# Kernel optimization log

Measured on AMD Instinct MI355X. Metric: run time of the kernel, lower is better.

## Reference

```python
import jax, jax.numpy as jnp
import numpy as np

SCALE = 0.08838834764831845  # 1/sqrt(head_dim=128)
B, H, HKV, D = 32, 32, 8, 128
NUM_BLOCKS, BLOCK_SIZE, MAX_NUM_BLOCKS = 4096, 16, 256


def setup_inputs() -> dict:
    key = jax.random.key(0)
    ks = jax.random.split(key, 8)
    q = jax.random.normal(ks[0], (B, H, D), dtype=jnp.float32)
    k = jax.random.normal(ks[1], (B, HKV, D), dtype=jnp.float32)
    v = jax.random.normal(ks[2], (B, HKV, D), dtype=jnp.float32)
    k_cache = jax.random.normal(ks[3], (NUM_BLOCKS, BLOCK_SIZE, HKV, D), dtype=jnp.float32)
    v_cache = jax.random.normal(ks[4], (NUM_BLOCKS, BLOCK_SIZE, HKV, D), dtype=jnp.float32)
    slot_mapping = jax.random.randint(ks[5], (B,), 0, NUM_BLOCKS * BLOCK_SIZE, dtype=jnp.int32)
    block_tables = jax.random.randint(ks[6], (B, MAX_NUM_BLOCKS), 0, NUM_BLOCKS, dtype=jnp.int32)
    context_lens = jax.random.randint(ks[7], (B,), 0, MAX_NUM_BLOCKS * BLOCK_SIZE, dtype=jnp.int32)
    return {"q": q, "k": k, "v": v, "k_cache": k_cache, "v_cache": v_cache,
            "slot_mapping": slot_mapping, "block_tables": block_tables,
            "context_lens": context_lens}


def reference(q, k, v, k_cache, v_cache, slot_mapping, block_tables, context_lens):
    nb, bs, hkv, d = k_cache.shape
    b, h, _ = q.shape
    groups = h // hkv  # GQA repeat factor (repeat_interleave semantics)

    # --- store_kvcache: scatter the new decode token's k/v into the paged cache ---
    k_cache = k_cache.reshape(-1, hkv, d).at[slot_mapping].set(k).reshape(nb, bs, hkv, d)
    v_cache = v_cache.reshape(-1, hkv, d).at[slot_mapping].set(v).reshape(nb, bs, hkv, d)

    # --- block-table gather: [B, max_blocks] -> [B, T, HKV, D], T = max_blocks*bs ---
    t = block_tables.shape[1] * bs
    ids = jnp.maximum(block_tables, 0)  # clamp_min(0)
    k_tok = k_cache[ids].reshape(b, t, hkv, d)
    v_tok = v_cache[ids].reshape(b, t, hkv, d)

    # --- validity mask: block must be >=0 and token position < context_len ---
    pos = jnp.arange(t, dtype=jnp.int32)
    block_mask = jnp.repeat(block_tables >= 0, bs, axis=1)  # [B, T]
    valid = block_mask & (pos[None, :] < context_lens[:, None])
    has_tokens = valid.any(axis=1)  # [B]
    safe_valid = valid | ((~has_tokens)[:, None] & (pos[None, :] == 0))

    # --- attention (GQA via reshape instead of repeat_interleave materialization) ---
    qg = q.reshape(b, hkv, groups, d)  # head h = kv*groups + g matches repeat_interleave
    scores = jnp.einsum('bkgd,btkd->bkgt', qg, k_tok) * SCALE  # [B, HKV, G, T]
    scores = jnp.where(safe_valid[:, None, None, :], scores, -jnp.inf)
    w = jax.nn.softmax(scores.astype(jnp.float32), axis=-1).astype(q.dtype)
    o = jnp.einsum('bkgt,btkd->bkgd', w, v_tok).reshape(b, h, d)
    o = o * has_tokens[:, None, None].astype(o.dtype)
    return o[:, None, :, :]  # [B, 1, H, D] (matches transpose(1,2) of [B,H,1,D])
```

## Files before the change

### kernel.cpp

```cpp
#include <hip/hip_runtime.h>
#include <math.h>

#define B_ 32
#define H_ 32
#define HKV_ 8
#define G_ 4
#define D_ 128
#define BS_ 16
#define MAXNB_ 256
#define NPAGES_ 4096
#define NSLOTS_ (NPAGES_ * BS_)
#define SC_ (0.08838834764831845f * 1.4426950408889634f)
#define NEG_ -1e30f

__global__ void build_slot_map(const int* __restrict__ slot_mapping,
                               unsigned char* __restrict__ map,
                               unsigned int* __restrict__ pagemask) {
  const int tid = threadIdx.x;
  uint4* m4 = (uint4*)map;
#pragma unroll
  for (int i = 0; i < NSLOTS_ / 16 / 256; ++i)
    m4[tid + i * 256] = make_uint4(0u, 0u, 0u, 0u);
  uint4* p4 = (uint4*)pagemask;
#pragma unroll
  for (int i = 0; i < NPAGES_ * 4 / 16 / 256; ++i)
    p4[tid + i * 256] = make_uint4(0u, 0u, 0u, 0u);
  __syncthreads();
  if (tid == 0) {
#pragma unroll
    for (int j = 0; j < B_; ++j) {
      int s = slot_mapping[j];
      map[s] = (unsigned char)(j + 1);
      pagemask[s >> 4] |= (1u << (s & 15));
    }
  }
}

__global__ __launch_bounds__(256, 2) void attn_split(
    const float* __restrict__ q,
    const float* __restrict__ k_new,
    const float* __restrict__ v_new,
    const float* __restrict__ k_cache,
    const float* __restrict__ v_cache,
    const int* __restrict__ block_tables,
    const int* __restrict__ context_lens,
    const unsigned char* __restrict__ map,
    const unsigned int* __restrict__ pagemask,
    float* __restrict__ O_part,
    float* __restrict__ M_part,
    float* __restrict__ L_part,
    int nsplit)
{
  __shared__ float Ml[4][4];
  __shared__ float Ll[4][4];
  __shared__ float Ob[4][4][128];

  const int tid = threadIdx.x;
  const int tok = tid >> 4;
  const int c = tid & 15;

  const int s  = blockIdx.x % nsplit;
  const int bk = blockIdx.x / nsplit;
  const int kv = bk % HKV_;
  const int b  = bk / HKV_;

  float qr[G_][8];
#pragma unroll
  for (int g = 0; g < G_; ++g) {
    const float* qp = q + ((size_t)(b * H_ + kv * G_ + g)) * D_ + c * 8;
    float4 a0 = *(const float4*)qp;
    float4 a1 = *(const float4*)(qp + 4);
    qr[g][0] = a0.x * SC_; qr[g][1] = a0.y * SC_;
    qr[g][2] = a0.z * SC_; qr[g][3] = a0.w * SC_;
    qr[g][4] = a1.x * SC_; qr[g][5] = a1.y * SC_;
    qr[g][6] = a1.z * SC_; qr[g][7] = a1.w * SC_;
  }

  float m2[G_], l[G_], o[G_][8];
#pragma unroll
  for (int g = 0; g < G_; ++g) {
    m2[g] = NEG_; l[g] = 0.f;
#pragma unroll
    for (int j = 0; j < 8; ++j) o[g][j] = 0.f;
  }

  const int ctx = context_lens[b];
  const int pages_total = (ctx + BS_ - 1) / BS_;
  const int p_per = (pages_total + nsplit - 1) / nsplit;
  const int p0 = s * p_per;
  const int p1 = min(p0 + p_per, pages_total);

  const int toff = tok * (HKV_ * D_) + kv * D_ + c * 8;

  float4 pk0, pk1, pv0, pv1;
  int pblk = 0;
  unsigned int pmsk = 0;

  if (p0 < p1) {
    pblk = block_tables[b * MAXNB_ + p0];
    int bc = pblk < 0 ? 0 : pblk;
    pmsk = pagemask[bc];
    const float* kp = k_cache + (size_t)bc * (BS_ * HKV_ * D_) + toff;
    const float* vp = v_cache + (size_t)bc * (BS_ * HKV_ * D_) + toff;
    pk0 = *(const float4*)kp;
    pk1 = *(const float4*)(kp + 4);
    pv0 = *(const float4*)vp;
    pv1 = *(const float4*)(vp + 4);
  }

  for (int pg = p0; pg < p1; ++pg) {
    float4 k0 = pk0, k1 = pk1, v0 = pv0, v1 = pv1;
    const int this_blk = pblk;
    const unsigned int this_msk = pmsk;

    if (pg + 1 < p1) {
      pblk = block_tables[b * MAXNB_ + pg + 1];
      int bc = pblk < 0 ? 0 : pblk;
      pmsk = pagemask[bc];
      const float* kp = k_cache + (size_t)bc * (BS_ * HKV_ * D_) + toff;
      const float* vp = v_cache + (size_t)bc * (BS_ * HKV_ * D_) + toff;
      pk0 = *(const float4*)kp;
      pk1 = *(const float4*)(kp + 4);
      pv0 = *(const float4*)vp;
      pv1 = *(const float4*)(vp + 4);
    }

    if (this_msk != 0) {
      int bc = this_blk < 0 ? 0 : this_blk;
      int mj = map[bc * BS_ + tok];
      if (mj != 0) {
        const int j = mj - 1;
        const float* kp = k_new + ((size_t)(j * HKV_ + kv)) * D_ + c * 8;
        const float* vp = v_new + ((size_t)(j * HKV_ + kv)) * D_ + c * 8;
        k0 = *(const float4*)kp; k1 = *(const float4*)(kp + 4);
        v0 = *(const float4*)vp; v1 = *(const float4*)(vp + 4);
      }
    }

    float dt[G_];
#pragma unroll
    for (int g = 0; g < G_; ++g) {
      dt[g] = qr[g][0] * k0.x + qr[g][1] * k0.y + qr[g][2] * k0.z + qr[g][3] * k0.w
            + qr[g][4] * k1.x + qr[g][5] * k1.y + qr[g][6] * k1.z + qr[g][7] * k1.w;
    }
#pragma unroll
    for (int off = 1; off < 16; off <<= 1) {
#pragma unroll
      for (int g = 0; g < G_; ++g) dt[g] += __shfl_xor(dt[g], off, 16);
    }
    const int pos = pg * BS_ + tok;
    if ((pos < ctx) && (this_blk >= 0)) {
#pragma unroll
      for (int g = 0; g < G_; ++g) {
        float t2 = dt[g];
        float mn = fmaxf(m2[g], t2);
        float al = exp2f(m2[g] - mn);
        float p  = exp2f(t2 - mn);
        l[g] = l[g] * al + p;
        m2[g] = mn;
        o[g][0] = o[g][0] * al + p * v0.x;
        o[g][1] = o[g][1] * al + p * v0.y;
        o[g][2] = o[g][2] * al + p * v0.z;
        o[g][3] = o[g][3] * al + p * v0.w;
        o[g][4] = o[g][4] * al + p * v1.x;
        o[g][5] = o[g][5] * al + p * v1.y;
        o[g][6] = o[g][6] * al + p * v1.z;
        o[g][7] = o[g][7] * al + p * v1.w;
      }
    }
  }

#pragma unroll
  for (int off = 16; off < 64; off <<= 1) {
#pragma unroll
    for (int g = 0; g < G_; ++g) {
      float mo = __shfl_xor(m2[g], off, 64);
      float lo = __shfl_xor(l[g], off, 64);
      float mn = fmaxf(m2[g], mo);
      float f1 = exp2f(m2[g] - mn);
      float f2 = exp2f(mo - mn);
      l[g] = f1 * l[g] + f2 * lo;
      m2[g] = mn;
#pragma unroll
      for (int j = 0; j < 8; ++j)
        o[g][j] = f1 * o[g][j] + f2 * __shfl_xor(o[g][j], off, 64);
    }
  }

  const int w = tid >> 6;
  if ((tid & 63) == 0) {
#pragma unroll
    for (int g = 0; g < G_; ++g) { Ml[w][g] = m2[g]; Ll[w][g] = l[g]; }
  }
  if (((tid >> 4) & 3) == 0) {
#pragma unroll
    for (int g = 0; g < G_; ++g) {
      float* dst = &Ob[w][g][c * 8];
      *(float4*)dst       = make_float4(o[g][0], o[g][1], o[g][2], o[g][3]);
      *(float4*)(dst + 4) = make_float4(o[g][4], o[g][5], o[g][6], o[g][7]);
    }
  }
  __syncthreads();

  const int g2 = tid >> 6;
  const int dd = (tid & 63) * 2;
  float M = NEG_;
#pragma unroll
  for (int wv = 0; wv < 4; ++wv) M = fmaxf(M, Ml[wv][g2]);
  float Ls = 0.f, a0 = 0.f, a1 = 0.f;
#pragma unroll
  for (int wv = 0; wv < 4; ++wv) {
    float f = exp2f(Ml[wv][g2] - M);
    Ls += f * Ll[wv][g2];
    float2 ov = *(const float2*)&Ob[wv][g2][dd];
    a0 += f * ov.x;
    a1 += f * ov.y;
  }
  const size_t pi = ((size_t)((b * HKV_ + kv) * G_ + g2) * nsplit + s);
  O_part[pi * D_ + dd]     = a0;
  O_part[pi * D_ + dd + 1] = a1;
  if (dd == 0) { M_part[pi] = M; L_part[pi] = Ls; }
}

__global__ void combine_splits(const float* __restrict__ O_part,
                               const float* __restrict__ M_part,
                               const float* __restrict__ L_part,
                               const int* __restrict__ context_lens,
                               float* __restrict__ out, int nsplit) {
  const int blk = blockIdx.x;
  const int b = blk >> 5;
  const int d = threadIdx.x;
  const int ctx = context_lens[b];
  float r = 0.f;
  if (ctx > 0) {
    const size_t base = (size_t)blk * nsplit;
    float M = NEG_;
    for (int s = 0; s < nsplit; ++s) M = fmaxf(M, M_part[base + s]);
    float den = 0.f, acc = 0.f;
    for (int s = 0; s < nsplit; ++s) {
      float f = exp2f(M_part[base + s] - M);
      den += f * L_part[base + s];
      acc += f * O_part[(base + s) * D_ + d];
    }
    r = den > 0.f ? acc / den : 0.f;
  }
  out[(size_t)blk * D_ + d] = r;
}

extern "C" void kernel_launch(void* const* d_in, const int* in_sizes, int n_in,
                              void* d_out, int out_size, void* d_ws, size_t ws_size,
                              hipStream_t stream) {
  const float* q = (const float*)d_in[0];
  const float* k = (const float*)d_in[1];
  const float* v = (const float*)d_in[2];
  const float* k_cache = (const float*)d_in[3];
  const float* v_cache = (const float*)d_in[4];
  const int* slot_mapping = (const int*)d_in[5];
  const int* block_tables = (const int*)d_in[6];
  const int* context_lens = (const int*)d_in[7];
  float* out = (float*)d_out;

  const size_t map_bytes = NSLOTS_;
  const size_t pmask_bytes = NPAGES_ * sizeof(unsigned int);
  unsigned char* map = (unsigned char*)d_ws;
  unsigned int* pagemask = (unsigned int*)((char*)d_ws + map_bytes);

  int nsplit = 16;
  while (nsplit > 1) {
    size_t need = map_bytes + pmask_bytes +
                  (size_t)B_ * HKV_ * G_ * nsplit * (D_ + 2) * sizeof(float);
    if (need <= ws_size) break;
    nsplit >>= 1;
  }
  float* O_part = (float*)((char*)d_ws + map_bytes + pmask_bytes);
  float* M_part = O_part + (size_t)B_ * HKV_ * G_ * nsplit * D_;
  float* L_part = M_part + (size_t)B_ * HKV_ * G_ * nsplit;

  build_slot_map<<<1, 256, 0, stream>>>(slot_mapping, map, pagemask);
  attn_split<<<B_ * HKV_ * nsplit, 256, 0, stream>>>(
      q, k, v, k_cache, v_cache, block_tables, context_lens, map, pagemask,
      O_part, M_part, L_part, nsplit);
  combine_splits<<<B_ * H_, D_, 0, stream>>>(O_part, M_part, L_part,
                                             context_lens, out, nsplit);
}
```

Measured before the change: 515.6 us.

## Double-buffer page loads and precompute per-sequence overwrite bitmask

The attention loop now keeps two page buffers in flight and reloads each buffer's K right after its dot product and its V right after the softmax update, so memory latency overlaps more compute. A per-sequence bitmask of pages hit by the new-token scatter is built in the setup kernel, which removes the dependent pagemask load from the inner loop. Launch bounds are raised to 4 blocks per SM to increase occupancy. The costs are a serial pass over the block tables with atomics in the single-block setup kernel and more register pressure that could cause spills.

Result: slower. 537.2 us (+4.2%).

```diff
diff --git a/kernel.cpp b/kernel.cpp
--- a/kernel.cpp
+++ b/kernel.cpp
@@ -10,12 +10,16 @@
 #define MAXNB_ 256
 #define NPAGES_ 4096
 #define NSLOTS_ (NPAGES_ * BS_)
+#define PGSZ_ (BS_ * HKV_ * D_)
+#define OVW_ 10
 #define SC_ (0.08838834764831845f * 1.4426950408889634f)
 #define NEG_ -1e30f
 
 __global__ void build_slot_map(const int* __restrict__ slot_mapping,
+                               const int* __restrict__ block_tables,
                                unsigned char* __restrict__ map,
-                               unsigned int* __restrict__ pagemask) {
+                               unsigned int* __restrict__ pagemask,
+                               unsigned int* __restrict__ ovr) {
   const int tid = threadIdx.x;
   uint4* m4 = (uint4*)map;
 #pragma unroll
@@ -25,6 +29,7 @@
 #pragma unroll
   for (int i = 0; i < NPAGES_ * 4 / 16 / 256; ++i)
     p4[tid + i * 256] = make_uint4(0u, 0u, 0u, 0u);
+  for (int i = tid; i < B_ * OVW_; i += 256) ovr[i] = 0u;
   __syncthreads();
   if (tid == 0) {
 #pragma unroll
@@ -34,9 +39,18 @@
       pagemask[s >> 4] |= (1u << (s & 15));
     }
   }
+  __syncthreads();
+  for (int e = tid; e < B_ * MAXNB_; e += 256) {
+    int pgid = block_tables[e];
+    if (pgid >= 0 && pgid < NPAGES_ && pagemask[pgid] != 0u) {
+      int bb = e >> 8;
+      int pos = e & 255;
+      atomicOr(&ovr[bb * OVW_ + (pos >> 5)], 1u << (pos & 31));
+    }
+  }
 }
 
-__global__ __launch_bounds__(256, 2) void attn_split(
+__global__ __launch_bounds__(256, 4) void attn_split(
     const float* __restrict__ q,
     const float* __restrict__ k_new,
     const float* __restrict__ v_new,
@@ -45,7 +59,7 @@
     const int* __restrict__ block_tables,
     const int* __restrict__ context_lens,
     const unsigned char* __restrict__ map,
-    const unsigned int* __restrict__ pagemask,
+    const unsigned int* __restrict__ ovr,
     float* __restrict__ O_part,
     float* __restrict__ M_part,
     float* __restrict__ L_part,
@@ -91,65 +105,64 @@
   const int p1 = min(p0 + p_per, pages_total);
 
   const int toff = tok * (HKV_ * D_) + kv * D_ + c * 8;
-
-  float4 pk0, pk1, pv0, pv1;
-  int pblk = 0;
-  unsigned int pmsk = 0;
-
-  if (p0 < p1) {
-    pblk = block_tables[b * MAXNB_ + p0];
-    int bc = pblk < 0 ? 0 : pblk;
-    pmsk = pagemask[bc];
-    const float* kp = k_cache + (size_t)bc * (BS_ * HKV_ * D_) + toff;
-    const float* vp = v_cache + (size_t)bc * (BS_ * HKV_ * D_) + toff;
-    pk0 = *(const float4*)kp;
-    pk1 = *(const float4*)(kp + 4);
-    pv0 = *(const float4*)vp;
-    pv1 = *(const float4*)(vp + 4);
-  }
-
-  for (int pg = p0; pg < p1; ++pg) {
-    float4 k0 = pk0, k1 = pk1, v0 = pv0, v1 = pv1;
-    const int this_blk = pblk;
-    const unsigned int this_msk = pmsk;
-
-    if (pg + 1 < p1) {
-      pblk = block_tables[b * MAXNB_ + pg + 1];
-      int bc = pblk < 0 ? 0 : pblk;
-      pmsk = pagemask[bc];
-      const float* kp = k_cache + (size_t)bc * (BS_ * HKV_ * D_) + toff;
-      const float* vp = v_cache + (size_t)bc * (BS_ * HKV_ * D_) + toff;
-      pk0 = *(const float4*)kp;
-      pk1 = *(const float4*)(kp + 4);
-      pv0 = *(const float4*)vp;
-      pv1 = *(const float4*)(vp + 4);
-    }
-
-    if (this_msk != 0) {
-      int bc = this_blk < 0 ? 0 : this_blk;
-      int mj = map[bc * BS_ + tok];
+  const int bt_base = b * MAXNB_;
+
+  unsigned long long dwr;
+  if (p_per <= 32) {
+    const unsigned int* ow = ovr + b * OVW_;
+    const int i0 = p0 >> 5, s0 = p0 & 31;
+    unsigned long long lo = ow[i0], hi = ow[i0 + 1];
+    dwr = ((hi << 32) | lo) >> s0;
+  } else {
+    dwr = ~0ull;
+  }
+
+  struct PBuf { float4 k0, k1, v0, v1; int blk; };
+  PBuf A, B;
+
+  auto fill = [&](PBuf& P, int id, bool ok) {
+    P.blk = id;
+    const int nb = id < 0 ? 0 : id;
+    const float* kp = k_cache + (size_t)nb * PGSZ_ + toff;
+    const float* vp = v_cache + (size_t)nb * PGSZ_ + toff;
+    if (ok) {
+      P.k0 = *(const float4*)kp; P.k1 = *(const float4*)(kp + 4);
+      P.v0 = *(const float4*)vp; P.v1 = *(const float4*)(vp + 4);
+    } else {
+      P.k0 = P.k1 = P.v0 = P.v1 = make_float4(0.f, 0.f, 0.f, 0.f);
+    }
+  };
+
+  auto step = [&](PBuf& P, int pgx, int nid, bool filln, bool chk) {
+    const int thisblk = P.blk;
+    if (chk) {
+      const int bc0 = thisblk < 0 ? 0 : thisblk;
+      const int mj = map[bc0 * BS_ + tok];
       if (mj != 0) {
         const int j = mj - 1;
         const float* kp = k_new + ((size_t)(j * HKV_ + kv)) * D_ + c * 8;
         const float* vp = v_new + ((size_t)(j * HKV_ + kv)) * D_ + c * 8;
-        k0 = *(const float4*)kp; k1 = *(const float4*)(kp + 4);
-        v0 = *(const float4*)vp; v1 = *(const float4*)(vp + 4);
+        P.k0 = *(const float4*)kp; P.k1 = *(const float4*)(kp + 4);
+        P.v0 = *(const float4*)vp; P.v1 = *(const float4*)(vp + 4);
       }
     }
-
     float dt[G_];
 #pragma unroll
     for (int g = 0; g < G_; ++g) {
-      dt[g] = qr[g][0] * k0.x + qr[g][1] * k0.y + qr[g][2] * k0.z + qr[g][3] * k0.w
-            + qr[g][4] * k1.x + qr[g][5] * k1.y + qr[g][6] * k1.z + qr[g][7] * k1.w;
-    }
+      dt[g] = qr[g][0] * P.k0.x + qr[g][1] * P.k0.y + qr[g][2] * P.k0.z + qr[g][3] * P.k0.w
+            + qr[g][4] * P.k1.x + qr[g][5] * P.k1.y + qr[g][6] * P.k1.z + qr[g][7] * P.k1.w;
+    }
+    const int nb = nid < 0 ? 0 : nid;
+    const float* nkp = k_cache + (size_t)nb * PGSZ_ + toff;
+    const float* nvp = v_cache + (size_t)nb * PGSZ_ + toff;
+    if (filln) { P.k0 = *(const float4*)nkp; P.k1 = *(const float4*)(nkp + 4); }
 #pragma unroll
     for (int off = 1; off < 16; off <<= 1) {
 #pragma unroll
       for (int g = 0; g < G_; ++g) dt[g] += __shfl_xor(dt[g], off, 16);
     }
-    const int pos = pg * BS_ + tok;
-    if ((pos < ctx) && (this_blk >= 0)) {
+    const int pos = pgx * BS_ + tok;
+    if ((pos < ctx) && (thisblk >= 0)) {
 #pragma unroll
       for (int g = 0; g < G_; ++g) {
         float t2 = dt[g];
@@ -158,17 +171,38 @@
         float p  = exp2f(t2 - mn);
         l[g] = l[g] * al + p;
         m2[g] = mn;
-        o[g][0] = o[g][0] * al + p * v0.x;
-        o[g][1] = o[g][1] * al + p * v0.y;
-        o[g][2] = o[g][2] * al + p * v0.z;
-        o[g][3] = o[g][3] * al + p * v0.w;
-        o[g][4] = o[g][4] * al + p * v1.x;
-        o[g][5] = o[g][5] * al + p * v1.y;
-        o[g][6] = o[g][6] * al + p * v1.z;
-        o[g][7] = o[g][7] * al + p * v1.w;
+        o[g][0] = o[g][0] * al + p * P.v0.x;
+        o[g][1] = o[g][1] * al + p * P.v0.y;
+        o[g][2] = o[g][2] * al + p * P.v0.z;
+        o[g][3] = o[g][3] * al + p * P.v0.w;
+        o[g][4] = o[g][4] * al + p * P.v1.x;
+        o[g][5] = o[g][5] * al + p * P.v1.y;
+        o[g][6] = o[g][6] * al + p * P.v1.z;
+        o[g][7] = o[g][7] * al + p * P.v1.w;
       }
     }
-  }
+    if (filln) { P.v0 = *(const float4*)nvp; P.v1 = *(const float4*)(nvp + 4); }
+    P.blk = nid;
+  };
+
+  {
+    int i0 = (p0 < p1) ? block_tables[bt_base + p0] : 0;
+    int i1 = (p0 + 1 < p1) ? block_tables[bt_base + p0 + 1] : 0;
+    fill(A, i0, p0 < p1);
+    fill(B, i1, p0 + 1 < p1);
+  }
+  int nidA = (p0 + 2 < p1) ? block_tables[bt_base + p0 + 2] : 0;
+  int nidB = (p0 + 3 < p1) ? block_tables[bt_base + p0 + 3] : 0;
+
+  int pg = p0;
+  for (; pg + 1 < p1; pg += 2) {
+    step(A, pg,     nidA, pg + 2 < p1, (dwr & 1ull) != 0);
+    step(B, pg + 1, nidB, pg + 3 < p1, (dwr & 2ull) != 0);
+    nidA = (pg + 4 < p1) ? block_tables[bt_base + pg + 4] : 0;
+    nidB = (pg + 5 < p1) ? block_tables[bt_base + pg + 5] : 0;
+    dwr >>= 2;
+  }
+  if (pg < p1) step(A, pg, 0, false, (dwr & 1ull) != 0);
 
 #pragma unroll
   for (int off = 16; off < 64; off <<= 1) {
@@ -262,23 +296,26 @@
 
   const size_t map_bytes = NSLOTS_;
   const size_t pmask_bytes = NPAGES_ * sizeof(unsigned int);
+  const size_t ovr_bytes = 2048;
   unsigned char* map = (unsigned char*)d_ws;
   unsigned int* pagemask = (unsigned int*)((char*)d_ws + map_bytes);
+  unsigned int* ovr = (unsigned int*)((char*)d_ws + map_bytes + pmask_bytes);
 
   int nsplit = 16;
   while (nsplit > 1) {
-    size_t need = map_bytes + pmask_bytes +
+    size_t need = map_bytes + pmask_bytes + ovr_bytes +
                   (size_t)B_ * HKV_ * G_ * nsplit * (D_ + 2) * sizeof(float);
     if (need <= ws_size) break;
     nsplit >>= 1;
   }
-  float* O_part = (float*)((char*)d_ws + map_bytes + pmask_bytes);
+  float* O_part = (float*)((char*)d_ws + map_bytes + pmask_bytes + ovr_bytes);
   float* M_part = O_part + (size_t)B_ * HKV_ * G_ * nsplit * D_;
   float* L_part = M_part + (size_t)B_ * HKV_ * G_ * nsplit;
 
-  build_slot_map<<<1, 256, 0, stream>>>(slot_mapping, map, pagemask);
+  build_slot_map<<<1, 256, 0, stream>>>(slot_mapping, block_tables,
+                                        map, pagemask, ovr);
   attn_split<<<B_ * HKV_ * nsplit, 256, 0, stream>>>(
-      q, k, v, k_cache, v_cache, block_tables, context_lens, map, pagemask,
+      q, k, v, k_cache, v_cache, block_tables, context_lens, map, ovr,
       O_part, M_part, L_part, nsplit);
   combine_splits<<<B_ * H_, D_, 0, stream>>>(O_part, M_part, L_part,
                                              context_lens, out, nsplit);
```
